# Kernel optimization log

Measured on AMD Instinct MI355X. Metric: run time of the kernel, lower is better.

## Reference

```python
import jax, jax.numpy as jnp
import numpy as np

NB, B, IN, HID = 8, 256, 512, 512
G = 4 * HID
WB, IB, ABNM = 8, 8, 8
NL = 0.05


def quant(x, bits, r):
    # QuantFunc.forward: scale, clamp to (-1+1/step, 1-1/step), round to step grid, rescale
    step = 2.0 ** (bits - 1)
    x01 = jnp.clip(x / r, -1.0 + 1.0 / step, 1.0 - 1.0 / step)
    return jnp.round(x01 * step) / step * r


def pact(x, a):
    # pact_a_bmm vectorized over the block dim: sign(x)*0.5*(|x| - ||x|-a| + a)
    a3 = a[:, None, None]
    return jnp.sign(x) * 0.5 * (jnp.abs(x) - jnp.abs(jnp.abs(x) - a3) + a3)


def custom_mm(inp, w, b, nw, nb):
    # CustomMM_bmm.forward: quantize weights/bias (range 1.0), add scaled noise, bmm
    wq = quant(w, WB, 1.0)
    bq = quant(b, WB, 1.0)
    out = jnp.einsum('bni,bio->bno', inp, wq + nw * jnp.max(w) * NL)
    return out + bq + nb * jnp.max(b) * NL


def setup_inputs():
    key = jax.random.key(0)
    ks = jax.random.split(key, 11)
    inp = {
        'input': jax.random.normal(ks[0], (B, IN), jnp.float32),
        'hx': jax.random.normal(ks[1], (NB, B, HID), jnp.float32),
        'cx': jax.random.normal(ks[2], (NB, B, HID), jnp.float32),
        'weight_ih': jax.random.normal(ks[3], (NB, IN, G), jnp.float32),
        'weight_hh': jax.random.normal(ks[4], (NB, HID, G), jnp.float32),
        'bias_ih': jax.random.normal(ks[5], (NB, 1, G), jnp.float32),
        'bias_hh': jax.random.normal(ks[6], (NB, 1, G), jnp.float32),
        'noise_wih': jax.random.normal(ks[7], (NB, IN, G), jnp.float32),
        'noise_whh': jax.random.normal(ks[8], (NB, HID, G), jnp.float32),
        'noise_bih': jax.random.normal(ks[9], (NB, 1, G), jnp.float32),
        'noise_bhh': jax.random.normal(ks[10], (NB, 1, G), jnp.float32),
        'a1': jnp.full((NB,), 128.0, jnp.float32),
        'a3': jnp.ones((NB,), jnp.float32),
        'a4': jnp.ones((NB,), jnp.float32),
        'a5': jnp.ones((NB,), jnp.float32),
        'a6': jnp.ones((NB,), jnp.float32),
        'a7': jnp.full((NB,), 4.0, jnp.float32),
        'a8': jnp.ones((NB,), jnp.float32),
        'a9': jnp.full((NB,), 4.0, jnp.float32),
        'a10': jnp.ones((NB,), jnp.float32),
        'a11': jnp.full((NB,), 4.0, jnp.float32),
    }
    return inp


def reference(input, hx, cx, weight_ih, weight_hh, bias_ih, bias_hh,
              noise_wih, noise_whh, noise_bih, noise_bhh,
              a1, a3, a4, a5, a6, a7, a8, a9, a10, a11):
    xr = jnp.broadcast_to(input[None], (NB,) + input.shape)  # input.repeat(n_blocks,1,1)
    xq = quant(pact(xr, a1), IB, a1[:, None, None])
    gates = custom_mm(xq, weight_ih, bias_ih, noise_wih, noise_bih) \
          + custom_mm(hx, weight_hh, bias_hh, noise_whh, noise_bhh)
    i, j, f, o = jnp.split(gates, 4, axis=2)
    qp = lambda x, a: quant(pact(x, a), ABNM, a[:, None, None])
    fg = qp(jax.nn.sigmoid(f), a3)
    ig = qp(jax.nn.sigmoid(i), a4)
    act = qp(jnp.tanh(j), a5)
    og = qp(jax.nn.sigmoid(o), a6)
    gated = qp(cx * fg, a7)
    actin = qp(ig * act, a8)
    new_c = qp(gated + actin, a9)
    actc = qp(jnp.tanh(new_c), a10)
    new_h = qp(actc * og, a11)
    return new_h, new_c
```

## Files before the change

kernel.cpp:

```cpp
#include <hip/hip_runtime.h>
#include <hip/hip_bf16.h>

#define NBATCH 8
#define BROWS 256
#define KDIM 512
#define HIDD 512
#define GDIM 2048
#define KSTEP 64
#define NIT (KDIM / KSTEP)

typedef float f32x4 __attribute__((ext_vector_type(4)));
typedef __bf16 bf16x8 __attribute__((ext_vector_type(8)));

__device__ __forceinline__ unsigned fenc(float f) {
    unsigned u = __float_as_uint(f);
    return (u & 0x80000000u) ? ~u : (u | 0x80000000u);
}
__device__ __forceinline__ float fdec(unsigned e) {
    unsigned u = (e & 0x80000000u) ? (e & 0x7fffffffu) : ~e;
    return __uint_as_float(u);
}
__device__ __forceinline__ unsigned umaxu(unsigned a, unsigned b) { return a > b ? a : b; }

__device__ __forceinline__ float qpact(float x, float a) {
    float ax = fabsf(x);
    float p  = copysignf(0.5f * (ax - fabsf(ax - a) + a), x);
    float x01 = p / a;
    x01 = fminf(fmaxf(x01, -0.9921875f), 0.9921875f);
    return (rintf(x01 * 128.f) * 0.0078125f) * a;
}
__device__ __forceinline__ float q1(float x) {
    float x01 = fminf(fmaxf(x, -0.9921875f), 0.9921875f);
    return rintf(x01 * 128.f) * 0.0078125f;
}
__device__ __forceinline__ float sigmf(float x) { return 1.0f / (1.0f + expf(-x)); }

__global__ void k_init(unsigned* m) { if (threadIdx.x < 4) m[threadIdx.x] = 0u; }

__global__ void k_max(const float* __restrict__ w_ih, const float* __restrict__ w_hh,
                      const float* __restrict__ b_ih, const float* __restrict__ b_hh,
                      unsigned* __restrict__ omax) {
    int which = blockIdx.y;
    const float* src = which == 0 ? w_ih : which == 1 ? w_hh : which == 2 ? b_ih : b_hh;
    int n4 = (which < 2 ? NBATCH * KDIM * GDIM : NBATCH * GDIM) >> 2;
    unsigned best = 0u;
    int stride = gridDim.x * blockDim.x;
    for (int i = blockIdx.x * blockDim.x + threadIdx.x; i < n4; i += stride) {
        float4 v = ((const float4*)src)[i];
        best = umaxu(best, fenc(v.x)); best = umaxu(best, fenc(v.y));
        best = umaxu(best, fenc(v.z)); best = umaxu(best, fenc(v.w));
    }
    #pragma unroll
    for (int off = 32; off > 0; off >>= 1)
        best = umaxu(best, (unsigned)__shfl_down((int)best, off, 64));
    __shared__ unsigned red[4];
    int lane = threadIdx.x & 63, wv = threadIdx.x >> 6;
    if (lane == 0) red[wv] = best;
    __syncthreads();
    if (threadIdx.x == 0) {
        unsigned b2 = umaxu(umaxu(red[0], red[1]), umaxu(red[2], red[3]));
        atomicMax(&omax[which], b2);
    }
}

__global__ void k_prep(const float* __restrict__ input, const float* __restrict__ hx,
                       const float* __restrict__ bih, const float* __restrict__ bhh,
                       const float* __restrict__ nbih, const float* __restrict__ nbhh,
                       const float* __restrict__ a1, const unsigned* __restrict__ maxes,
                       __hip_bfloat16* __restrict__ xqh, __hip_bfloat16* __restrict__ hxh,
                       __hip_bfloat16* __restrict__ hxl, float* __restrict__ bias_comb) {
    const int NX = NBATCH * BROWS * KDIM;
    const int NH = NBATCH * BROWS * HIDD;
    const int NBC = NBATCH * GDIM;
    int total = NX + NH + NBC;
    int stride = gridDim.x * blockDim.x;
    for (int i = blockIdx.x * blockDim.x + threadIdx.x; i < total; i += stride) {
        if (i < NX) {
            int nb = i >> 17;
            int rem = i & 131071;
            float v = qpact(input[rem], a1[nb]);
            xqh[i] = __float2bfloat16(v);
        } else if (i < NX + NH) {
            int j = i - NX;
            float h = hx[j];
            __hip_bfloat16 hi = __float2bfloat16(h);
            hxh[j] = hi;
            hxl[j] = __float2bfloat16(h - __bfloat162float(hi));
        } else {
            int j = i - NX - NH;
            float mb_ih = fdec(maxes[2]);
            float mb_hh = fdec(maxes[3]);
            bias_comb[j] = q1(bih[j]) + (nbih[j] * mb_ih) * 0.05f
                         + q1(bhh[j]) + (nbhh[j] * mb_hh) * 0.05f;
        }
    }
}

__global__ __launch_bounds__(1024, 1) void k_gemm(
    const float* __restrict__ w_ih, const float* __restrict__ w_hh,
    const float* __restrict__ n_ih, const float* __restrict__ n_hh,
    const __hip_bfloat16* __restrict__ xqh, const __hip_bfloat16* __restrict__ hxh,
    const __hip_bfloat16* __restrict__ hxl,
    const float* __restrict__ bias_comb, const float* __restrict__ cx,
    const float* __restrict__ a3, const float* __restrict__ a4, const float* __restrict__ a5,
    const float* __restrict__ a6, const float* __restrict__ a7, const float* __restrict__ a8,
    const float* __restrict__ a9, const float* __restrict__ a10, const float* __restrict__ a11,
    const unsigned* __restrict__ maxes,
    float* __restrict__ out_h, float* __restrict__ out_c)
{
    __shared__ __hip_bfloat16 Bsm[2][4][64][72];

    int tid = threadIdx.x;
    int lane = tid & 63, wv = tid >> 6;
    int nb = blockIdx.x & 7;
    int cb = blockIdx.x >> 3;

    const float* wih_b = w_ih + nb * KDIM * GDIM;
    const float* whh_b = w_hh + nb * KDIM * GDIM;
    const float* nih_b = n_ih + nb * KDIM * GDIM;
    const float* nhh_b = n_hh + nb * KDIM * GDIM;
    const __hip_bfloat16* xq_b = xqh + nb * BROWS * KDIM;
    const __hip_bfloat16* hh_b = hxh + nb * BROWS * KDIM;
    const __hip_bfloat16* hl_b = hxl + nb * BROWS * KDIM;

    float c_ih = fdec(maxes[0]);
    float c_hh = fdec(maxes[1]);

    f32x4 acc[4] = {};

    int lh = lane & 15;
    int g  = lane >> 4;
    int arow = (wv << 4) + lh;

    int c  = tid & 15;
    int kk = tid >> 4;

    float rw1a[4], rz1a[4], rw2a[4], rz2a[4];
    float rw1b[4], rz1b[4], rw2b[4], rz2b[4];

#define STAGE(R1, Z1, R2, Z2, K0) {                          \
    int base = ((K0) + kk) * GDIM + (cb << 4) + c;           \
    _Pragma("unroll")                                        \
    for (int nf = 0; nf < 4; ++nf) {                         \
        int gx = base + (nf << 9);                           \
        R1[nf] = wih_b[gx]; Z1[nf] = nih_b[gx];              \
        R2[nf] = whh_b[gx]; Z2[nf] = nhh_b[gx];              \
    } }

#define CVT(P, R1, Z1, R2, Z2) {                             \
    _Pragma("unroll")                                        \
    for (int nf = 0; nf < 4; ++nf) {                         \
        int n = (nf << 4) + c;                               \
        float w1 = R1[nf], z1 = Z1[nf];                      \
        float wq1 = rintf(fminf(fmaxf(w1, -0.9921875f), 0.9921875f) * 128.f) * 0.0078125f; \
        float e1 = wq1 + (z1 * c_ih) * 0.05f;                \
        __hip_bfloat16 h1 = __float2bfloat16(e1);            \
        Bsm[P][0][n][kk] = h1;                               \
        Bsm[P][1][n][kk] = __float2bfloat16(e1 - __bfloat162float(h1)); \
        float w2 = R2[nf], z2 = Z2[nf];                      \
        float wq2 = rintf(fminf(fmaxf(w2, -0.9921875f), 0.9921875f) * 128.f) * 0.0078125f; \
        float e2 = wq2 + (z2 * c_hh) * 0.05f;                \
        __hip_bfloat16 h2 = __float2bfloat16(e2);            \
        Bsm[P][2][n][kk] = h2;                               \
        Bsm[P][3][n][kk] = __float2bfloat16(e2 - __bfloat162float(h2)); \
    } }

#define COMPUTE(P, K0) {                                     \
    _Pragma("unroll")                                        \
    for (int kf = 0; kf < 2; ++kf) {                         \
        int ko = (K0) + (kf << 5) + (g << 3);                \
        int kb = (kf << 5) + (g << 3);                       \
        bf16x8 ax = *(const bf16x8*)(xq_b + arow * KDIM + ko); \
        bf16x8 ah = *(const bf16x8*)(hh_b + arow * KDIM + ko); \
        bf16x8 al = *(const bf16x8*)(hl_b + arow * KDIM + ko); \
        _Pragma("unroll")                                    \
        for (int nf = 0; nf < 4; ++nf) {                     \
            int n = (nf << 4) + lh;                          \
            bf16x8 b0 = *(const bf16x8*)&Bsm[P][0][n][kb];   \
            bf16x8 b1 = *(const bf16x8*)&Bsm[P][1][n][kb];   \
            bf16x8 b2 = *(const bf16x8*)&Bsm[P][2][n][kb];   \
            bf16x8 b3 = *(const bf16x8*)&Bsm[P][3][n][kb];   \
            acc[nf] = __builtin_amdgcn_mfma_f32_16x16x32_bf16(ax, b0, acc[nf], 0, 0, 0); \
            acc[nf] = __builtin_amdgcn_mfma_f32_16x16x32_bf16(ax, b1, acc[nf], 0, 0, 0); \
            acc[nf] = __builtin_amdgcn_mfma_f32_16x16x32_bf16(ah, b2, acc[nf], 0, 0, 0); \
            acc[nf] = __builtin_amdgcn_mfma_f32_16x16x32_bf16(ah, b3, acc[nf], 0, 0, 0); \
            acc[nf] = __builtin_amdgcn_mfma_f32_16x16x32_bf16(al, b2, acc[nf], 0, 0, 0); \
        } \
    } }

    STAGE(rw1a, rz1a, rw2a, rz2a, 0);
    STAGE(rw1b, rz1b, rw2b, rz2b, KSTEP);

    for (int it = 0; it < NIT; it += 2) {
        CVT(0, rw1a, rz1a, rw2a, rz2a);
        if (it + 2 < NIT) STAGE(rw1a, rz1a, rw2a, rz2a, (it + 2) * KSTEP);
        __syncthreads();
        COMPUTE(0, it * KSTEP);
        CVT(1, rw1b, rz1b, rw2b, rz2b);
        if (it + 3 < NIT) STAGE(rw1b, rz1b, rw2b, rz2b, (it + 3) * KSTEP);
        __syncthreads();
        COMPUTE(1, (it + 1) * KSTEP);
    }

    int hcol = (cb << 4) + lh;
    float A3 = a3[nb], A4 = a4[nb], A5 = a5[nb], A6 = a6[nb], A7 = a7[nb];
    float A8 = a8[nb], A9 = a9[nb], A10 = a10[nb], A11 = a11[nb];
    float bc_i = bias_comb[nb * GDIM + hcol];
    float bc_j = bias_comb[nb * GDIM + 512 + hcol];
    float bc_f = bias_comb[nb * GDIM + 1024 + hcol];
    float bc_o = bias_comb[nb * GDIM + 1536 + hcol];
    #pragma unroll
    for (int rg = 0; rg < 4; ++rg) {
        int r = (wv << 4) + (g << 2) + rg;
        float gi = acc[0][rg] + bc_i;
        float gj = acc[1][rg] + bc_j;
        float gf = acc[2][rg] + bc_f;
        float go = acc[3][rg] + bc_o;
        float fg = qpact(sigmf(gf), A3);
        float ig = qpact(sigmf(gi), A4);
        float act = qpact(tanhf(gj), A5);
        float og = qpact(sigmf(go), A6);
        int oidx = (nb * BROWS + r) * HIDD + hcol;
        float cv = cx[oidx];
        float gated = qpact(cv * fg, A7);
        float actin = qpact(ig * act, A8);
        float ncv = qpact(gated + actin, A9);
        float acv = qpact(tanhf(ncv), A10);
        float nhv = qpact(acv * og, A11);
        out_h[oidx] = nhv;
        out_c[oidx] = ncv;
    }
}

extern "C" void kernel_launch(void* const* d_in, const int* in_sizes, int n_in,
                              void* d_out, int out_size, void* d_ws, size_t ws_size,
                              hipStream_t stream) {
    const float* input = (const float*)d_in[0];
    const float* hx    = (const float*)d_in[1];
    const float* cx    = (const float*)d_in[2];
    const float* w_ih  = (const float*)d_in[3];
    const float* w_hh  = (const float*)d_in[4];
    const float* b_ih  = (const float*)d_in[5];
    const float* b_hh  = (const float*)d_in[6];
    const float* n_wih = (const float*)d_in[7];
    const float* n_whh = (const float*)d_in[8];
    const float* n_bih = (const float*)d_in[9];
    const float* n_bhh = (const float*)d_in[10];
    const float* a1  = (const float*)d_in[11];
    const float* a3  = (const float*)d_in[12];
    const float* a4  = (const float*)d_in[13];
    const float* a5  = (const float*)d_in[14];
    const float* a6  = (const float*)d_in[15];
    const float* a7  = (const float*)d_in[16];
    const float* a8  = (const float*)d_in[17];
    const float* a9  = (const float*)d_in[18];
    const float* a10 = (const float*)d_in[19];
    const float* a11 = (const float*)d_in[20];

    float* out_h = (float*)d_out;
    float* out_c = out_h + NBATCH * BROWS * HIDD;

    char* ws = (char*)d_ws;
    unsigned* maxes = (unsigned*)ws;
    __hip_bfloat16* xqh = (__hip_bfloat16*)(ws + 256);
    __hip_bfloat16* hxh = (__hip_bfloat16*)(ws + 256 + 2097152);
    __hip_bfloat16* hxl = (__hip_bfloat16*)(ws + 256 + 2 * 2097152);
    float* bias_comb    = (float*)(ws + 256 + 3 * 2097152);

    k_init<<<1, 64, 0, stream>>>(maxes);
    k_max<<<dim3(256, 4), 256, 0, stream>>>(w_ih, w_hh, b_ih, b_hh, maxes);
    k_prep<<<2048, 256, 0, stream>>>(input, hx, b_ih, b_hh, n_bih, n_bhh, a1, maxes,
                                     xqh, hxh, hxl, bias_comb);
    k_gemm<<<NBATCH * 32, 1024, 0, stream>>>(w_ih, w_hh, n_wih, n_whh, xqh, hxh, hxl,
                                             bias_comb, cx,
                                             a3, a4, a5, a6, a7, a8, a9, a10, a11,
                                             maxes, out_h, out_c);
}
```

Baseline: 85.15 us.

## Restructure weight staging to per-thread k-octets with vectorized LDS stores and early A loads

Each thread now stages 8 consecutive k values for one column of one matrix (ih or hh, chosen by thread index), so converted hi/lo bf16 values are packed and written to shared memory as 16-byte vectors instead of scattered 2-byte stores. The A-operand fragments are loaded before the conversion step and pinned with an empty asm, so global latency overlaps the CVT work. Global weight reads become less coalesced per instruction (stride over k rows), and the thread-to-matrix mapping assumes at least 1024 threads.

After: 85.49 us. Within noise of the previous version (+0.4%).

```diff
diff --git a/kernel.cpp b/kernel.cpp
--- a/kernel.cpp
+++ b/kernel.cpp
@@ -132,74 +132,93 @@
     int g  = lane >> 4;
     int arow = (wv << 4) + lh;
 
-    int c  = tid & 15;
-    int kk = tid >> 4;
-
-    float rw1a[4], rz1a[4], rw2a[4], rz2a[4];
-    float rw1b[4], rz1b[4], rw2b[4], rz2b[4];
-
-#define STAGE(R1, Z1, R2, Z2, K0) {                          \
-    int base = ((K0) + kk) * GDIM + (cb << 4) + c;           \
+    int sn   = tid & 63;
+    int soct = (tid >> 6) & 7;
+    int shh  = tid >> 9;
+    const float* wsrc = shh ? whh_b : wih_b;
+    const float* zsrc = shh ? nhh_b : nih_b;
+    float cmax = shh ? c_hh : c_ih;
+    int matHi = shh << 1;
+    int scol = ((sn >> 4) << 9) + (cb << 4) + (sn & 15);
+
+    float rwa[8], rza[8], rwb[8], rzb[8];
+    bf16x8 ax0, ax1, ah0, ah1, al0, al1;
+
+#define STAGE(RW, RZ, K0) {                                  \
+    int kb = (K0) + (soct << 3);                             \
+    _Pragma("unroll")                                        \
+    for (int j = 0; j < 8; ++j) {                            \
+        int gx = (kb + j) * GDIM + scol;                     \
+        RW[j] = wsrc[gx]; RZ[j] = zsrc[gx];                  \
+    } }
+
+#define ALOAD(K0) {                                          \
+    int a0 = arow * KDIM + (K0) + (g << 3);                  \
+    ax0 = *(const bf16x8*)(xq_b + a0);                       \
+    ax1 = *(const bf16x8*)(xq_b + a0 + 32);                  \
+    ah0 = *(const bf16x8*)(hh_b + a0);                       \
+    ah1 = *(const bf16x8*)(hh_b + a0 + 32);                  \
+    al0 = *(const bf16x8*)(hl_b + a0);                       \
+    al1 = *(const bf16x8*)(hl_b + a0 + 32);                  \
+    asm volatile("" :: "v"(__builtin_bit_cast(f32x4, ax0)), "v"(__builtin_bit_cast(f32x4, ax1)), \
+                       "v"(__builtin_bit_cast(f32x4, ah0)), "v"(__builtin_bit_cast(f32x4, ah1)), \
+                       "v"(__builtin_bit_cast(f32x4, al0)), "v"(__builtin_bit_cast(f32x4, al1))); }
+
+#define CVT(P, RW, RZ) {                                     \
+    bf16x8 hi8, lo8;                                         \
+    _Pragma("unroll")                                        \
+    for (int j = 0; j < 8; ++j) {                            \
+        float w = RW[j];                                     \
+        float wq = rintf(fminf(fmaxf(w, -0.9921875f), 0.9921875f) * 128.f) * 0.0078125f; \
+        float e = wq + (RZ[j] * cmax) * 0.05f;               \
+        __hip_bfloat16 h = __float2bfloat16(e);              \
+        float lo = e - __bfloat162float(h);                  \
+        __hip_bfloat16 l = __float2bfloat16(lo);             \
+        hi8[j] = *reinterpret_cast<__bf16*>(&h);             \
+        lo8[j] = *reinterpret_cast<__bf16*>(&l);             \
+    }                                                        \
+    *(bf16x8*)&Bsm[P][matHi][sn][soct << 3] = hi8;           \
+    *(bf16x8*)&Bsm[P][matHi + 1][sn][soct << 3] = lo8; }
+
+#define COMPUTE(P) {                                         \
     _Pragma("unroll")                                        \
     for (int nf = 0; nf < 4; ++nf) {                         \
-        int gx = base + (nf << 9);                           \
-        R1[nf] = wih_b[gx]; Z1[nf] = nih_b[gx];              \
-        R2[nf] = whh_b[gx]; Z2[nf] = nhh_b[gx];              \
+        int n = (nf << 4) + lh;                              \
+        int kb0 = g << 3, kb1 = 32 + kb0;                    \
+        bf16x8 b0 = *(const bf16x8*)&Bsm[P][0][n][kb0];      \
+        bf16x8 b1 = *(const bf16x8*)&Bsm[P][1][n][kb0];      \
+        bf16x8 b2 = *(const bf16x8*)&Bsm[P][2][n][kb0];      \
+        bf16x8 b3 = *(const bf16x8*)&Bsm[P][3][n][kb0];      \
+        acc[nf] = __builtin_amdgcn_mfma_f32_16x16x32_bf16(ax0, b0, acc[nf], 0, 0, 0); \
+        acc[nf] = __builtin_amdgcn_mfma_f32_16x16x32_bf16(ax0, b1, acc[nf], 0, 0, 0); \
+        acc[nf] = __builtin_amdgcn_mfma_f32_16x16x32_bf16(ah0, b2, acc[nf], 0, 0, 0); \
+        acc[nf] = __builtin_amdgcn_mfma_f32_16x16x32_bf16(ah0, b3, acc[nf], 0, 0, 0); \
+        acc[nf] = __builtin_amdgcn_mfma_f32_16x16x32_bf16(al0, b2, acc[nf], 0, 0, 0); \
+        b0 = *(const bf16x8*)&Bsm[P][0][n][kb1];             \
+        b1 = *(const bf16x8*)&Bsm[P][1][n][kb1];             \
+        b2 = *(const bf16x8*)&Bsm[P][2][n][kb1];             \
+        b3 = *(const bf16x8*)&Bsm[P][3][n][kb1];             \
+        acc[nf] = __builtin_amdgcn_mfma_f32_16x16x32_bf16(ax1, b0, acc[nf], 0, 0, 0); \
+        acc[nf] = __builtin_amdgcn_mfma_f32_16x16x32_bf16(ax1, b1, acc[nf], 0, 0, 0); \
+        acc[nf] = __builtin_amdgcn_mfma_f32_16x16x32_bf16(ah1, b2, acc[nf], 0, 0, 0); \
+        acc[nf] = __builtin_amdgcn_mfma_f32_16x16x32_bf16(ah1, b3, acc[nf], 0, 0, 0); \
+        acc[nf] = __builtin_amdgcn_mfma_f32_16x16x32_bf16(al1, b2, acc[nf], 0, 0, 0); \
     } }
 
-#define CVT(P, R1, Z1, R2, Z2) {                             \
-    _Pragma("unroll")                                        \
-    for (int nf = 0; nf < 4; ++nf) {                         \
-        int n = (nf << 4) + c;                               \
-        float w1 = R1[nf], z1 = Z1[nf];                      \
-        float wq1 = rintf(fminf(fmaxf(w1, -0.9921875f), 0.9921875f) * 128.f) * 0.0078125f; \
-        float e1 = wq1 + (z1 * c_ih) * 0.05f;                \
-        __hip_bfloat16 h1 = __float2bfloat16(e1);            \
-        Bsm[P][0][n][kk] = h1;                               \
-        Bsm[P][1][n][kk] = __float2bfloat16(e1 - __bfloat162float(h1)); \
-        float w2 = R2[nf], z2 = Z2[nf];                      \
-        float wq2 = rintf(fminf(fmaxf(w2, -0.9921875f), 0.9921875f) * 128.f) * 0.0078125f; \
-        float e2 = wq2 + (z2 * c_hh) * 0.05f;                \
-        __hip_bfloat16 h2 = __float2bfloat16(e2);            \
-        Bsm[P][2][n][kk] = h2;                               \
-        Bsm[P][3][n][kk] = __float2bfloat16(e2 - __bfloat162float(h2)); \
-    } }
-
-#define COMPUTE(P, K0) {                                     \
-    _Pragma("unroll")                                        \
-    for (int kf = 0; kf < 2; ++kf) {                         \
-        int ko = (K0) + (kf << 5) + (g << 3);                \
-        int kb = (kf << 5) + (g << 3);                       \
-        bf16x8 ax = *(const bf16x8*)(xq_b + arow * KDIM + ko); \
-        bf16x8 ah = *(const bf16x8*)(hh_b + arow * KDIM + ko); \
-        bf16x8 al = *(const bf16x8*)(hl_b + arow * KDIM + ko); \
-        _Pragma("unroll")                                    \
-        for (int nf = 0; nf < 4; ++nf) {                     \
-            int n = (nf << 4) + lh;                          \
-            bf16x8 b0 = *(const bf16x8*)&Bsm[P][0][n][kb];   \
-            bf16x8 b1 = *(const bf16x8*)&Bsm[P][1][n][kb];   \
-            bf16x8 b2 = *(const bf16x8*)&Bsm[P][2][n][kb];   \
-            bf16x8 b3 = *(const bf16x8*)&Bsm[P][3][n][kb];   \
-            acc[nf] = __builtin_amdgcn_mfma_f32_16x16x32_bf16(ax, b0, acc[nf], 0, 0, 0); \
-            acc[nf] = __builtin_amdgcn_mfma_f32_16x16x32_bf16(ax, b1, acc[nf], 0, 0, 0); \
-            acc[nf] = __builtin_amdgcn_mfma_f32_16x16x32_bf16(ah, b2, acc[nf], 0, 0, 0); \
-            acc[nf] = __builtin_amdgcn_mfma_f32_16x16x32_bf16(ah, b3, acc[nf], 0, 0, 0); \
-            acc[nf] = __builtin_amdgcn_mfma_f32_16x16x32_bf16(al, b2, acc[nf], 0, 0, 0); \
-        } \
-    } }
-
-    STAGE(rw1a, rz1a, rw2a, rz2a, 0);
-    STAGE(rw1b, rz1b, rw2b, rz2b, KSTEP);
+    STAGE(rwa, rza, 0);
+    STAGE(rwb, rzb, KSTEP);
 
     for (int it = 0; it < NIT; it += 2) {
-        CVT(0, rw1a, rz1a, rw2a, rz2a);
-        if (it + 2 < NIT) STAGE(rw1a, rz1a, rw2a, rz2a, (it + 2) * KSTEP);
+        ALOAD(it * KSTEP);
+        CVT(0, rwa, rza);
+        if (it + 2 < NIT) STAGE(rwa, rza, (it + 2) * KSTEP);
         __syncthreads();
-        COMPUTE(0, it * KSTEP);
-        CVT(1, rw1b, rz1b, rw2b, rz2b);
-        if (it + 3 < NIT) STAGE(rw1b, rz1b, rw2b, rz2b, (it + 3) * KSTEP);
+        COMPUTE(0);
+        ALOAD((it + 1) * KSTEP);
+        CVT(1, rwb, rzb);
+        if (it + 3 < NIT) STAGE(rwb, rzb, (it + 3) * KSTEP);
         __syncthreads();
-        COMPUTE(1, (it + 1) * KSTEP);
+        COMPUTE(1);
     }
 
     int hcol = (cb << 4) + lh;
```
